# Kernel tuning notes

Measured on AMD Instinct MI355X. Metric: run time of the kernel, lower is better.

The kernel has to match this reference:

```python
import jax, jax.numpy as jnp
import numpy as np

N_NODES = 100000
N_EDGES = 1600000
N_FEAT = 128
N_HID = 128
N_CLASS = 10
N_GRAPHS = 512
BN_EPS = 1e-5


def setup_inputs() -> dict:
    key = jax.random.key(0)
    ks = jax.random.split(key, 12)
    x = jax.random.normal(ks[0], (N_NODES, N_FEAT), dtype=jnp.float32)
    edge_index = jax.random.randint(ks[1], (2, N_EDGES), 0, N_NODES, dtype=jnp.int32)
    batch = jnp.sort(jax.random.randint(ks[2], (N_NODES,), 0, N_GRAPHS, dtype=jnp.int32))
    s1 = 1.0 / np.sqrt(N_FEAT)
    s2 = 1.0 / np.sqrt(N_HID)
    W1 = jax.random.uniform(ks[3], (N_FEAT, N_HID), jnp.float32, -s1, s1)
    b1 = jax.random.uniform(ks[4], (N_HID,), jnp.float32, -s1, s1)
    gamma = jnp.ones((N_HID,), jnp.float32)
    beta = jnp.zeros((N_HID,), jnp.float32)
    W2 = jax.random.uniform(ks[5], (N_HID, N_HID), jnp.float32, -s2, s2)
    b2 = jax.random.uniform(ks[6], (N_HID,), jnp.float32, -s2, s2)
    clsW = jax.random.uniform(ks[7], (N_HID, N_CLASS), jnp.float32, -s2, s2)
    clsb = jax.random.uniform(ks[8], (N_CLASS,), jnp.float32, -s2, s2)
    return {"x": x, "edge_index": edge_index, "batch": batch,
            "W1": W1, "b1": b1, "gamma": gamma, "beta": beta,
            "W2": W2, "b2": b2, "clsW": clsW, "clsb": clsb}


def _gcn_norm(edge_index, n_nodes):
    # add self-loops, compute symmetric normalization D^-1/2 A_hat D^-1/2
    loops = jnp.arange(n_nodes, dtype=edge_index.dtype)
    src = jnp.concatenate([edge_index[0], loops])
    dst = jnp.concatenate([edge_index[1], loops])
    deg = jax.ops.segment_sum(jnp.ones_like(dst, dtype=jnp.float32), dst,
                              num_segments=n_nodes)
    dinv = jnp.where(deg > 0, jax.lax.rsqrt(deg), 0.0)
    norm = dinv[src] * dinv[dst]  # [E + N]
    return src, dst, norm


def _gcn_conv(h, src, dst, norm, W, b, n_nodes):
    h = h @ W                                   # [N, nhid] dense GEMM
    msg = h[src] * norm[:, None]                # gather + scale  [E+N, nhid]
    out = jax.ops.segment_sum(msg, dst, num_segments=n_nodes)  # scatter-add
    return out + b


def reference(x, edge_index, batch, W1, b1, gamma, beta, W2, b2, clsW, clsb):
    n_nodes = x.shape[0]
    src, dst, norm = _gcn_norm(edge_index, n_nodes)
    # layer 1: GCNConv -> BatchNorm(eval, running stats 0/1) -> ReLU -> Dropout(eval=id)
    h = _gcn_conv(x, src, dst, norm, W1, b1, n_nodes)
    h = h * (gamma / jnp.sqrt(1.0 + BN_EPS)) + beta
    h = jax.nn.relu(h)
    # layer 2: GCNConv (output layer, no bn/act)
    h = _gcn_conv(h, src, dst, norm, W2, b2, n_nodes)
    # global mean pool over batch index
    sums = jax.ops.segment_sum(h, batch, num_segments=N_GRAPHS)          # [G, nhid]
    cnts = jax.ops.segment_sum(jnp.ones((n_nodes,), h.dtype), batch,
                               num_segments=N_GRAPHS)
    g = sums / jnp.maximum(cnts, 1.0)[:, None]
    out = jax.nn.log_softmax(g @ clsW + clsb, axis=1)                    # [G, nclass]
    return out, g
```

## Files before the change

kernel.cpp:

```cpp
#include <hip/hip_runtime.h>
#include <hip/hip_bf16.h>

#define N_NODES 100000
#define N_EDGES 1600000
#define N_FEAT 128
#define N_HID 128
#define N_CLASS 10
#define N_GRAPHS 512
#define BN_RSQRT 0.9999950000374997f

#define NRANGE 12500
#define NSUB 512
#define SCAP 640
#define HGROUP 32
#define BPB (NSUB / HGROUP)

#define XT_STRIDE 136
#define XT_BYTES (64 * XT_STRIDE * 2)
#define YW_STRIDE 36

typedef _Float16 half_t;
typedef __attribute__((ext_vector_type(2))) _Float16 half2v;
typedef __attribute__((ext_vector_type(4))) _Float16 half4v;
typedef __attribute__((ext_vector_type(8))) _Float16 half8v;
typedef __attribute__((ext_vector_type(4))) float floatx4;
typedef __attribute__((ext_vector_type(2))) float floatx2;

__global__ __launch_bounds__(256) void bucket_fused(
    const int* __restrict__ src, const int* __restrict__ dst,
    int* __restrict__ cnt, unsigned long long* __restrict__ bucketed,
    const float* __restrict__ W1, half_t* __restrict__ Wt1,
    const float* __restrict__ W2, half_t* __restrict__ Wt2,
    const int* __restrict__ batch, int* __restrict__ boffs,
    int chunkE, int E, int nnodes)
{
    __shared__ int wcnt[4][8];
    __shared__ int wbase[4][8];
    int blk = blockIdx.x;
    if (blk >= NSUB) {
        int k = blk - NSUB;
        if (k < 128) {
            int i = k * 256 + threadIdx.x;
            const float* W = (i < 16384) ? W1 : W2;
            half_t* Wt = (i < 16384) ? Wt1 : Wt2;
            int j = i & 16383;
            int c = j >> 7, kk = j & 127;
            Wt[(size_t)c * 128 + kk] = (half_t)W[(size_t)kk * 128 + c];
        } else {
            int i = (k - 128) * 256 + threadIdx.x;
            if (i < nnodes) {
                int b = batch[i];
                int prev = (i == 0) ? -1 : batch[i - 1];
                for (int g = prev + 1; g <= b; ++g) boffs[g] = i;
                if (i == nnodes - 1)
                    for (int g = b + 1; g <= N_GRAPHS; ++g) boffs[g] = nnodes;
            }
        }
        return;
    }
    int b = blk;
    int wave = threadIdx.x >> 6;
    int lane = threadIdx.x & 63;
    int e0 = b * chunkE;
    int e1 = e0 + chunkE < E ? e0 + chunkE : E;
    int iters = (chunkE + 255) / 256;

    int mycnt = 0;
    for (int it = 0; it < iters; ++it) {
        int e = e0 + it * 256 + threadIdx.x;
        bool valid = e < e1;
        int d = valid ? dst[e] : 0;
        int rr = (d * 8) / N_NODES;
#pragma unroll
        for (int r = 0; r < 8; ++r) {
            unsigned long long m = __ballot(valid && rr == r);
            if (lane == r) mycnt += __popcll(m);
        }
    }
    if (lane < 8) wcnt[wave][lane] = mycnt;
    __syncthreads();
    if (threadIdx.x < 8) {
        int r = threadIdx.x;
        int s = 0;
#pragma unroll
        for (int w = 0; w < 4; ++w) { wbase[w][r] = s; s += wcnt[w][r]; }
        cnt[r * NSUB + b] = s;
    }
    __syncthreads();

    int myoff = (lane < 8) ? wbase[wave][lane] : 0;
    for (int it = 0; it < iters; ++it) {
        int e = e0 + it * 256 + threadIdx.x;
        bool valid = e < e1;
        int s = valid ? src[e] : 0;
        int d = valid ? dst[e] : 0;
        int rr = (d * 8) / N_NODES;
        unsigned long long pk = ((unsigned long long)(unsigned)d << 32) | (unsigned)s;
#pragma unroll
        for (int r = 0; r < 8; ++r) {
            unsigned long long m = __ballot(valid && rr == r);
            int base_r = __shfl(myoff, r);
            if (valid && rr == r) {
                int pos = base_r + __popcll(m & ((1ull << lane) - 1));
                if (pos < SCAP)
                    bucketed[(size_t)(r * NSUB + b) * SCAP + pos] = pk;
            }
            if (lane == r) myoff += __popcll(m);
        }
    }
}

__global__ __launch_bounds__(256) void hist2(
    const unsigned long long* __restrict__ bucketed, const int* __restrict__ cnt,
    int* __restrict__ partial)
{
    __shared__ int h[NRANGE];
    int r = blockIdx.x & 7, g = blockIdx.x >> 3;
    for (int i = threadIdx.x; i < NRANGE; i += 256) h[i] = 0;
    __syncthreads();
    int rbase = r * NRANGE;
    for (int j = 0; j < BPB; ++j) {
        int b = g * BPB + j;
        int n = cnt[r * NSUB + b];
        if (n > SCAP) n = SCAP;
        const unsigned long long* seg = bucketed + (size_t)(r * NSUB + b) * SCAP;
        for (int i = threadIdx.x; i < n; i += 256)
            atomicAdd(&h[(int)(seg[i] >> 32) - rbase], 1);
    }
    __syncthreads();
    int* slice = partial + (size_t)(r * HGROUP + g) * NRANGE;
    for (int i = threadIdx.x; i < NRANGE; i += 256) slice[i] = h[i];
}

__global__ void deg_reduce(const int* __restrict__ partial, int* __restrict__ deg,
                           float* __restrict__ dinv, int* __restrict__ bsums, int n) {
    __shared__ int sm[256];
    int t = threadIdx.x;
    int i = blockIdx.x * 256 + t;
    int s = 0;
    if (i < n) {
        int rr = i / NRANGE;
        int dl = i - rr * NRANGE;
        const int* p = partial + (size_t)rr * HGROUP * NRANGE + dl;
#pragma unroll 8
        for (int g = 0; g < HGROUP; ++g) s += p[(size_t)g * NRANGE];
        deg[i] = s;
        dinv[i] = rsqrtf((float)s + 1.0f);
    }
    sm[t] = s;
    __syncthreads();
    for (int off = 128; off > 0; off >>= 1) {
        if (t < off) sm[t] += sm[t + off];
        __syncthreads();
    }
    if (t == 0) bsums[blockIdx.x] = sm[0];
}

__global__ void scan_small(int* __restrict__ bsums, int nb) {
    __shared__ int buf[1024];
    int t = threadIdx.x;
    int v = (t < nb) ? bsums[t] : 0;
    buf[t] = v;
    __syncthreads();
    for (int off = 1; off < 1024; off <<= 1) {
        int x = (t >= off) ? buf[t - off] : 0;
        __syncthreads();
        buf[t] += x;
        __syncthreads();
    }
    if (t < nb) bsums[t] = buf[t] - v;
}

__global__ __launch_bounds__(256) void scan_chunkoff(
    const int* __restrict__ in, const int* __restrict__ bsums,
    int* __restrict__ rowptr, int* __restrict__ partial, int n, int total)
{
    __shared__ int s[256];
    int t = threadIdx.x;
    int i = blockIdx.x * 256 + t;
    int v = (i < n) ? in[i] : 0;
    s[t] = v;
    __syncthreads();
    for (int off = 1; off < 256; off <<= 1) {
        int x = (t >= off) ? s[t - off] : 0;
        __syncthreads();
        s[t] += x;
        __syncthreads();
    }
    if (i == 0) rowptr[n] = total;
    if (i < n) {
        int excl = bsums[blockIdx.x] + s[t] - v;
        rowptr[i] = excl;
        int rr = i / NRANGE;
        int dl = i - rr * NRANGE;
        int* p = partial + (size_t)rr * HGROUP * NRANGE + dl;
        int vals[32];
#pragma unroll
        for (int g = 0; g < 32; ++g) vals[g] = p[(size_t)g * NRANGE];
        int running = excl;
#pragma unroll
        for (int g = 0; g < 32; ++g) {
            int tmp = vals[g];
            p[(size_t)g * NRANGE] = running;
            running += tmp;
        }
    }
}

__global__ __launch_bounds__(256, 4) void gemm1_mfma(
    const float* __restrict__ X, const half_t* __restrict__ Wt,
    const float* __restrict__ dinv, unsigned char* __restrict__ Y8, int nrows)
{
    __shared__ __align__(16) unsigned char smem[XT_BYTES];
    int tid = threadIdx.x;
    int r0base = blockIdx.x * 64;
    half_t* xt = (half_t*)smem;
    {
        const float4* xg = (const float4*)(X + (size_t)r0base * 128);
        if (r0base + 64 <= nrows) {
            float4 f[8];
#pragma unroll
            for (int j = 0; j < 8; ++j) f[j] = xg[j * 256 + tid];
#pragma unroll
            for (int j = 0; j < 8; ++j) {
                int idx = j * 256 + tid;
                int row = idx >> 5;
                int c4 = (idx & 31) << 2;
                half4v h = {(half_t)f[j].x, (half_t)f[j].y, (half_t)f[j].z, (half_t)f[j].w};
                *(half4v*)(xt + row * XT_STRIDE + c4) = h;
            }
        } else {
            int idxmax = (nrows - r0base) * 32;
#pragma unroll
            for (int j = 0; j < 8; ++j) {
                int idx = j * 256 + tid;
                if (idx < idxmax) {
                    float4 f = xg[idx];
                    int row = idx >> 5;
                    int c4 = (idx & 31) << 2;
                    half4v h = {(half_t)f.x, (half_t)f.y, (half_t)f.z, (half_t)f.w};
                    *(half4v*)(xt + row * XT_STRIDE + c4) = h;
                }
            }
        }
    }
    __syncthreads();
    int wave = tid >> 6;
    int lane = tid & 63;
    int n16  = lane & 15;
    int quad = lane >> 4;
    int r0 = r0base + wave * 16;
    bool active = r0 < nrows;
    int packedv[8];
    if (active) {
        int row = r0 + n16;
        const half_t* xr = xt + (wave * 16 + n16) * XT_STRIDE;
        half8v a0 = *(const half8v*)(xr + 0 * 32 + quad * 8);
        half8v a1 = *(const half8v*)(xr + 1 * 32 + quad * 8);
        half8v a2 = *(const half8v*)(xr + 2 * 32 + quad * 8);
        half8v a3 = *(const half8v*)(xr + 3 * 32 + quad * 8);
        float dr = dinv[row];
#pragma unroll
        for (int c = 0; c < 8; ++c) {
            const half8v* wrow = (const half8v*)(Wt + (size_t)(c * 16 + n16) * 128);
            floatx4 acc = {0.f, 0.f, 0.f, 0.f};
            acc = __builtin_amdgcn_mfma_f32_16x16x32_f16(wrow[0 * 4 + quad], a0, acc, 0, 0, 0);
            acc = __builtin_amdgcn_mfma_f32_16x16x32_f16(wrow[1 * 4 + quad], a1, acc, 0, 0, 0);
            acc = __builtin_amdgcn_mfma_f32_16x16x32_f16(wrow[2 * 4 + quad], a2, acc, 0, 0, 0);
            acc = __builtin_amdgcn_mfma_f32_16x16x32_f16(wrow[3 * 4 + quad], a3, acc, 0, 0, 0);
            int packed = __builtin_amdgcn_cvt_pk_fp8_f32(acc[0] * dr, acc[1] * dr, 0, false);
            packed = __builtin_amdgcn_cvt_pk_fp8_f32(acc[2] * dr, acc[3] * dr, packed, true);
            packedv[c] = packed;
        }
    }
    __syncthreads();
    int* yw = (int*)smem + wave * (16 * YW_STRIDE);
    if (active) {
#pragma unroll
        for (int c = 0; c < 8; ++c)
            yw[n16 * YW_STRIDE + c * 4 + quad] = packedv[c];
#pragma unroll
        for (int t = 0; t < 2; ++t) {
            int4 v = *(const int4*)(yw + (t * 8 + (lane >> 3)) * YW_STRIDE + (lane & 7) * 4);
            *(int4*)(Y8 + (size_t)r0 * 128 + t * 1024 + lane * 16) = v;
        }
    }
}

__global__ __launch_bounds__(256) void fill2(
    const unsigned long long* __restrict__ bucketed, const int* __restrict__ cnt,
    const int* __restrict__ partial, int* __restrict__ col)
{
    __shared__ int off[NRANGE];
    int r = blockIdx.x & 7, g = blockIdx.x >> 3;
    const int* slice = partial + (size_t)(r * HGROUP + g) * NRANGE;
    for (int i = threadIdx.x; i < NRANGE; i += 256) off[i] = slice[i];
    __syncthreads();
    int rbase = r * NRANGE;
    for (int j = 0; j < BPB; ++j) {
        int b = g * BPB + j;
        int n = cnt[r * NSUB + b];
        if (n > SCAP) n = SCAP;
        const unsigned long long* seg = bucketed + (size_t)(r * NSUB + b) * SCAP;
        for (int i = threadIdx.x; i < n; i += 256) {
            unsigned long long pk = seg[i];
            int pos = atomicAdd(&off[(int)(pk >> 32) - rbase], 1);
            col[pos] = (int)((unsigned)(pk & 0xffffffffu) << 7);
        }
    }
}

__global__ __launch_bounds__(256, 4) void gemm2_mfma(
    const half_t* __restrict__ X, const half_t* __restrict__ Wt,
    const float* __restrict__ dinv, unsigned char* __restrict__ Y8, int nrows)
{
    __shared__ __align__(16) unsigned char smem[XT_BYTES];
    int tid = threadIdx.x;
    int r0base = blockIdx.x * 64;
    half_t* xt = (half_t*)smem;
    {
        const half8v* xg = (const half8v*)(X + (size_t)r0base * 128);
        if (r0base + 64 <= nrows) {
            half8v v[4];
#pragma unroll
            for (int j = 0; j < 4; ++j) v[j] = xg[j * 256 + tid];
#pragma unroll
            for (int j = 0; j < 4; ++j) {
                int idx = j * 256 + tid;
                int row = idx >> 4;
                int sub = (idx & 15) << 3;
                *(half8v*)(xt + row * XT_STRIDE + sub) = v[j];
            }
        } else {
            int idxmax = (nrows - r0base) * 16;
#pragma unroll
            for (int j = 0; j < 4; ++j) {
                int idx = j * 256 + tid;
                if (idx < idxmax) {
                    half8v v = xg[idx];
                    int row = idx >> 4;
                    int sub = (idx & 15) << 3;
                    *(half8v*)(xt + row * XT_STRIDE + sub) = v;
                }
            }
        }
    }
    __syncthreads();
    int wave = tid >> 6;
    int lane = tid & 63;
    int n16  = lane & 15;
    int quad = lane >> 4;
    int r0 = r0base + wave * 16;
    bool active = r0 < nrows;
    int packedv[8];
    if (active) {
        int row = r0 + n16;
        const half_t* xr = xt + (wave * 16 + n16) * XT_STRIDE;
        half8v a0 = *(const half8v*)(xr + 0 * 32 + quad * 8);
        half8v a1 = *(const half8v*)(xr + 1 * 32 + quad * 8);
        half8v a2 = *(const half8v*)(xr + 2 * 32 + quad * 8);
        half8v a3 = *(const half8v*)(xr + 3 * 32 + quad * 8);
        float dr = dinv[row];
#pragma unroll
        for (int c = 0; c < 8; ++c) {
            const half8v* wrow = (const half8v*)(Wt + (size_t)(c * 16 + n16) * 128);
            floatx4 acc = {0.f, 0.f, 0.f, 0.f};
            acc = __builtin_amdgcn_mfma_f32_16x16x32_f16(wrow[0 * 4 + quad], a0, acc, 0, 0, 0);
            acc = __builtin_amdgcn_mfma_f32_16x16x32_f16(wrow[1 * 4 + quad], a1, acc, 0, 0, 0);
            acc = __builtin_amdgcn_mfma_f32_16x16x32_f16(wrow[2 * 4 + quad], a2, acc, 0, 0, 0);
            acc = __builtin_amdgcn_mfma_f32_16x16x32_f16(wrow[3 * 4 + quad], a3, acc, 0, 0, 0);
            int packed = __builtin_amdgcn_cvt_pk_fp8_f32(acc[0] * dr, acc[1] * dr, 0, false);
            packed = __builtin_amdgcn_cvt_pk_fp8_f32(acc[2] * dr, acc[3] * dr, packed, true);
            packedv[c] = packed;
        }
    }
    __syncthreads();
    int* yw = (int*)smem + wave * (16 * YW_STRIDE);
    if (active) {
#pragma unroll
        for (int c = 0; c < 8; ++c)
            yw[n16 * YW_STRIDE + c * 4 + quad] = packedv[c];
#pragma unroll
        for (int t = 0; t < 2; ++t) {
            int4 v = *(const int4*)(yw + (t * 8 + (lane >> 3)) * YW_STRIDE + (lane & 7) * 4);
            *(int4*)(Y8 + (size_t)r0 * 128 + t * 1024 + lane * 16) = v;
        }
    }
}

__global__ __launch_bounds__(256, 4) void agg_fp8(
    const unsigned char* __restrict__ hs, half_t* __restrict__ out,
    const int* __restrict__ col, const int* __restrict__ rowptr,
    const float* __restrict__ bias,
    const float* __restrict__ gamma, const float* __restrict__ beta,
    int nnodes, int do_bn_relu)
{
    int wave = threadIdx.x >> 6;
    int lane = threadIdx.x & 63;
    int q = lane >> 4;
    int l16 = lane & 15;
    int nb4 = (blockIdx.x * 4 + wave) * 4;
    int i = nb4 + q;
    bool valid = i < nnodes;
    unsigned iq = valid ? (unsigned)i : (unsigned)nnodes;
    unsigned f8 = (unsigned)l16 << 3;
    unsigned ZOFF = (unsigned)nnodes << 7;

    int e0 = valid ? rowptr[i] : 0;
    int e1 = valid ? rowptr[i + 1] : 0;
    int deg = e1 - e0;
    int m = deg;
    m = max(m, __shfl_xor(m, 16));
    m = max(m, __shfl_xor(m, 32));
    int nchunk = (m + 15) >> 4;

    unsigned long long us = *(const unsigned long long*)(hs + ((iq << 7) | f8));

    floatx2 a0 = {0.f, 0.f}, a1 = {0.f, 0.f}, a2 = {0.f, 0.f}, a3 = {0.f, 0.f};
    for (int t = 0; t < nchunk; ++t) {
        int idx = e0 + t * 16 + l16;
        unsigned cv = (idx < e1) ? (unsigned)col[idx] : ZOFF;
#pragma unroll
        for (int half = 0; half < 2; ++half) {
            const int kk = half * 8;
            unsigned long long v0, v1, v2, v3, v4, v5, v6, v7;
#define AGG_ADDR(K)                                                            \
            ({ unsigned sA = (unsigned)__builtin_amdgcn_readlane((int)cv, kk + K);      \
               unsigned sB = (unsigned)__builtin_amdgcn_readlane((int)cv, kk + K + 16); \
               unsigned sC = (unsigned)__builtin_amdgcn_readlane((int)cv, kk + K + 32); \
               unsigned sD = (unsigned)__builtin_amdgcn_readlane((int)cv, kk + K + 48); \
               unsigned rAB = (q & 1) ? sB : sA;                               \
               unsigned rCD = (q & 1) ? sD : sC;                               \
               unsigned rr = (q & 2) ? rCD : rAB;                              \
               *(const unsigned long long*)(hs + (rr | f8)); })
            v0 = AGG_ADDR(0);
            v1 = AGG_ADDR(1);
            v2 = AGG_ADDR(2);
            v3 = AGG_ADDR(3);
            v4 = AGG_ADDR(4);
            v5 = AGG_ADDR(5);
            v6 = AGG_ADDR(6);
            v7 = AGG_ADDR(7);
#undef AGG_ADDR
#define AGG_ACC(V)                                                             \
            { unsigned lo = (unsigned)(V), hi = (unsigned)((V) >> 32);         \
              a0 += __builtin_amdgcn_cvt_pk_f32_fp8((int)lo, false);           \
              a1 += __builtin_amdgcn_cvt_pk_f32_fp8((int)lo, true);            \
              a2 += __builtin_amdgcn_cvt_pk_f32_fp8((int)hi, false);           \
              a3 += __builtin_amdgcn_cvt_pk_f32_fp8((int)hi, true); }
            AGG_ACC(v0) AGG_ACC(v1) AGG_ACC(v2) AGG_ACC(v3)
            AGG_ACC(v4) AGG_ACC(v5) AGG_ACC(v6) AGG_ACC(v7)
#undef AGG_ACC
        }
    }
    {
        unsigned lo = (unsigned)us, hi = (unsigned)(us >> 32);
        a0 += __builtin_amdgcn_cvt_pk_f32_fp8((int)lo, false);
        a1 += __builtin_amdgcn_cvt_pk_f32_fp8((int)lo, true);
        a2 += __builtin_amdgcn_cvt_pk_f32_fp8((int)hi, false);
        a3 += __builtin_amdgcn_cvt_pk_f32_fp8((int)hi, true);
    }

    if (!valid) return;
    float di = rsqrtf((float)deg + 1.0f);
    int fbase = l16 * 8;
    float4 bi0 = *(const float4*)(bias + fbase);
    float4 bi1 = *(const float4*)(bias + fbase + 4);
    float o0 = fmaf(di, a0.x, bi0.x);
    float o1 = fmaf(di, a0.y, bi0.y);
    float o2 = fmaf(di, a1.x, bi0.z);
    float o3 = fmaf(di, a1.y, bi0.w);
    float o4 = fmaf(di, a2.x, bi1.x);
    float o5 = fmaf(di, a2.y, bi1.y);
    float o6 = fmaf(di, a3.x, bi1.z);
    float o7 = fmaf(di, a3.y, bi1.w);
    if (do_bn_relu) {
        float4 ga0 = *(const float4*)(gamma + fbase);
        float4 ga1 = *(const float4*)(gamma + fbase + 4);
        float4 be0 = *(const float4*)(beta + fbase);
        float4 be1 = *(const float4*)(beta + fbase + 4);
        o0 = fmaf(o0, ga0.x * BN_RSQRT, be0.x);
        o1 = fmaf(o1, ga0.y * BN_RSQRT, be0.y);
        o2 = fmaf(o2, ga0.z * BN_RSQRT, be0.z);
        o3 = fmaf(o3, ga0.w * BN_RSQRT, be0.w);
        o4 = fmaf(o4, ga1.x * BN_RSQRT, be1.x);
        o5 = fmaf(o5, ga1.y * BN_RSQRT, be1.y);
        o6 = fmaf(o6, ga1.z * BN_RSQRT, be1.z);
        o7 = fmaf(o7, ga1.w * BN_RSQRT, be1.w);
        o0 = o0 > 0.f ? o0 : 0.f;
        o1 = o1 > 0.f ? o1 : 0.f;
        o2 = o2 > 0.f ? o2 : 0.f;
        o3 = o3 > 0.f ? o3 : 0.f;
        o4 = o4 > 0.f ? o4 : 0.f;
        o5 = o5 > 0.f ? o5 : 0.f;
        o6 = o6 > 0.f ? o6 : 0.f;
        o7 = o7 > 0.f ? o7 : 0.f;
    }
    half8v ov = {(half_t)o0, (half_t)o1, (half_t)o2, (half_t)o3,
                 (half_t)o4, (half_t)o5, (half_t)o6, (half_t)o7};
    *(half8v*)(out + (size_t)i * 128 + fbase) = ov;
}

__global__ __launch_bounds__(512) void pool_cls(
    const half_t* __restrict__ h, const int* __restrict__ boffs,
    const float* __restrict__ clsW, const float* __restrict__ clsb,
    float* __restrict__ gout, float* __restrict__ out)
{
    __shared__ float red[8][128];
    __shared__ float zbuf[16];
    int g = blockIdx.x;
    int w = threadIdx.x >> 6;
    int lane = threadIdx.x & 63;
    int n0 = boffs[g], n1 = boffs[g + 1];
    float ax = 0.f, ay = 0.f;
    for (int n = n0 + w; n < n1; n += 8) {
        half2v v = *(const half2v*)(h + (size_t)n * 128 + lane * 2);
        ax += (float)v.x;
        ay += (float)v.y;
    }
    red[w][lane * 2] = ax;
    red[w][lane * 2 + 1] = ay;
    __syncthreads();
    if (w == 0) {
        float sx = 0.f, sy = 0.f;
#pragma unroll
        for (int j = 0; j < 8; ++j) {
            sx += red[j][lane * 2];
            sy += red[j][lane * 2 + 1];
        }
        float cnt = (float)((n1 - n0) > 1 ? (n1 - n0) : 1);
        float g0 = sx / cnt, g1 = sy / cnt;
        gout[(size_t)g * 128 + lane * 2] = g0;
        gout[(size_t)g * 128 + lane * 2 + 1] = g1;
        red[0][lane * 2] = g0;
        red[0][lane * 2 + 1] = g1;
    }
    __syncthreads();
    if (threadIdx.x < N_CLASS) {
        int c = threadIdx.x;
        float z = clsb[c];
        for (int k = 0; k < N_HID; ++k)
            z = fmaf(red[0][k], clsW[k * N_CLASS + c], z);
        zbuf[c] = z;
    }
    __syncthreads();
    if (threadIdx.x == 0) {
        float m = zbuf[0];
#pragma unroll
        for (int c = 1; c < N_CLASS; ++c) m = fmaxf(m, zbuf[c]);
        float s = 0.f;
#pragma unroll
        for (int c = 0; c < N_CLASS; ++c) s += expf(zbuf[c] - m);
        float l = logf(s);
#pragma unroll
        for (int c = 0; c < N_CLASS; ++c)
            out[(size_t)g * N_CLASS + c] = zbuf[c] - m - l;
    }
}

extern "C" void kernel_launch(void* const* d_in, const int* in_sizes, int n_in,
                              void* d_out, int out_size, void* d_ws, size_t ws_size,
                              hipStream_t stream) {
    const float* x     = (const float*)d_in[0];
    const int*   ei    = (const int*)d_in[1];
    const int*   batch = (const int*)d_in[2];
    const float* W1    = (const float*)d_in[3];
    const float* b1    = (const float*)d_in[4];
    const float* gamma = (const float*)d_in[5];
    const float* beta  = (const float*)d_in[6];
    const float* W2    = (const float*)d_in[7];
    const float* b2    = (const float*)d_in[8];
    const float* clsW  = (const float*)d_in[9];
    const float* clsb  = (const float*)d_in[10];

    const int N = in_sizes[0] / N_FEAT;
    const int E = in_sizes[1] / 2;
    const int* src = ei;
    const int* dst = ei + E;

    unsigned char* BA8 = (unsigned char*)d_ws;
    half_t* BB = (half_t*)(BA8 + (size_t)(N + 1) * 128);
    half_t* Wt1 = BB + (size_t)N * 128;
    half_t* Wt2 = Wt1 + 16384;
    int*   col     = (int*)(Wt2 + 16384);
    int*   rowptr  = col + E;
    int*   deg     = rowptr + (N + 4);
    float* dinv    = (float*)(deg + N);
    int*   cnt     = (int*)(dinv + N);
    unsigned long long* bucketed =
        (unsigned long long*)(cnt + 8 * NSUB);
    int*   partial = (int*)(bucketed + (size_t)8 * NSUB * SCAP);
    int*   boffs   = partial + 8 * HGROUP * NRANGE;
    int*   bsums   = boffs + N_GRAPHS + 4;

    const int nb = (N + 255) / 256;
    const int chunkE = (E + NSUB - 1) / NSUB;
    const int gemmBlocks = (N + 63) / 64;
    const int aggBlocks = (N + 15) / 16;

    hipMemsetAsync(BA8 + (size_t)N * 128, 0, 128, stream);

    bucket_fused<<<NSUB + 128 + nb, 256, 0, stream>>>(
        src, dst, cnt, bucketed, W1, Wt1, W2, Wt2, batch, boffs, chunkE, E, N);
    hist2<<<8 * HGROUP, 256, 0, stream>>>(bucketed, cnt, partial);
    deg_reduce<<<nb, 256, 0, stream>>>(partial, deg, dinv, bsums, N);
    scan_small<<<1, 1024, 0, stream>>>(bsums, nb);
    scan_chunkoff<<<nb, 256, 0, stream>>>(deg, bsums, rowptr, partial, N, E);
    gemm1_mfma<<<gemmBlocks, 256, 0, stream>>>(x, Wt1, dinv, BA8, N);
    fill2<<<256, 256, 0, stream>>>(bucketed, cnt, partial, col);
    agg_fp8<<<aggBlocks, 256, 0, stream>>>(BA8, BB, col, rowptr, b1, gamma, beta, N, 1);
    gemm2_mfma<<<gemmBlocks, 256, 0, stream>>>(BB, Wt2, dinv, BA8, N);
    agg_fp8<<<aggBlocks, 256, 0, stream>>>(BA8, BB, col, rowptr, b2, gamma, beta, N, 0);

    float* out = (float*)d_out;
    float* gsec = out + (size_t)N_GRAPHS * N_CLASS;
    pool_cls<<<N_GRAPHS, 512, 0, stream>>>(BB, boffs, clsW, clsb, gsec, out);
}
```

Baseline: 313.9 us.

## Replace bucketed CSR build with global atomic degree count and atomic fill

Drops the multi-pass bucket/histogram/partial-offset CSR construction. Degrees are now counted with global atomics on dst, and col is filled by atomically bumping per-node cursors. This removes the intermediate bucketed buffer and two kernels, plus their LDS histogram passes. In exchange it uses 1.6M global atomics twice with random addresses, and the order of neighbours within a row is no longer deterministic, so fp accumulation order may vary between runs.

```diff
diff --git a/kernel.cpp b/kernel.cpp
--- a/kernel.cpp
+++ b/kernel.cpp
@@ -9,12 +9,6 @@
 #define N_GRAPHS 512
 #define BN_RSQRT 0.9999950000374997f
 
-#define NRANGE 12500
-#define NSUB 512
-#define SCAP 640
-#define HGROUP 32
-#define BPB (NSUB / HGROUP)
-
 #define XT_STRIDE 136
 #define XT_BYTES (64 * XT_STRIDE * 2)
 #define YW_STRIDE 36
@@ -26,125 +20,55 @@
 typedef __attribute__((ext_vector_type(4))) float floatx4;
 typedef __attribute__((ext_vector_type(2))) float floatx2;
 
-__global__ __launch_bounds__(256) void bucket_fused(
-    const int* __restrict__ src, const int* __restrict__ dst,
-    int* __restrict__ cnt, unsigned long long* __restrict__ bucketed,
+__global__ __launch_bounds__(256) void count_fused(
+    const int* __restrict__ dst, int* __restrict__ deg,
     const float* __restrict__ W1, half_t* __restrict__ Wt1,
     const float* __restrict__ W2, half_t* __restrict__ Wt2,
     const int* __restrict__ batch, int* __restrict__ boffs,
-    int chunkE, int E, int nnodes)
-{
-    __shared__ int wcnt[4][8];
-    __shared__ int wbase[4][8];
+    int E, int nnodes, int EB)
+{
     int blk = blockIdx.x;
-    if (blk >= NSUB) {
-        int k = blk - NSUB;
-        if (k < 128) {
-            int i = k * 256 + threadIdx.x;
-            const float* W = (i < 16384) ? W1 : W2;
-            half_t* Wt = (i < 16384) ? Wt1 : Wt2;
-            int j = i & 16383;
-            int c = j >> 7, kk = j & 127;
-            Wt[(size_t)c * 128 + kk] = (half_t)W[(size_t)kk * 128 + c];
-        } else {
-            int i = (k - 128) * 256 + threadIdx.x;
-            if (i < nnodes) {
-                int b = batch[i];
-                int prev = (i == 0) ? -1 : batch[i - 1];
-                for (int g = prev + 1; g <= b; ++g) boffs[g] = i;
-                if (i == nnodes - 1)
-                    for (int g = b + 1; g <= N_GRAPHS; ++g) boffs[g] = nnodes;
-            }
+    if (blk < EB) {
+        int e4 = (blk * 256 + threadIdx.x) * 4;
+        if (e4 < E) {
+            int4 d4 = *(const int4*)(dst + e4);
+            atomicAdd(&deg[d4.x], 1);
+            atomicAdd(&deg[d4.y], 1);
+            atomicAdd(&deg[d4.z], 1);
+            atomicAdd(&deg[d4.w], 1);
         }
         return;
     }
-    int b = blk;
-    int wave = threadIdx.x >> 6;
-    int lane = threadIdx.x & 63;
-    int e0 = b * chunkE;
-    int e1 = e0 + chunkE < E ? e0 + chunkE : E;
-    int iters = (chunkE + 255) / 256;
-
-    int mycnt = 0;
-    for (int it = 0; it < iters; ++it) {
-        int e = e0 + it * 256 + threadIdx.x;
-        bool valid = e < e1;
-        int d = valid ? dst[e] : 0;
-        int rr = (d * 8) / N_NODES;
-#pragma unroll
-        for (int r = 0; r < 8; ++r) {
-            unsigned long long m = __ballot(valid && rr == r);
-            if (lane == r) mycnt += __popcll(m);
-        }
-    }
-    if (lane < 8) wcnt[wave][lane] = mycnt;
-    __syncthreads();
-    if (threadIdx.x < 8) {
-        int r = threadIdx.x;
-        int s = 0;
-#pragma unroll
-        for (int w = 0; w < 4; ++w) { wbase[w][r] = s; s += wcnt[w][r]; }
-        cnt[r * NSUB + b] = s;
-    }
-    __syncthreads();
-
-    int myoff = (lane < 8) ? wbase[wave][lane] : 0;
-    for (int it = 0; it < iters; ++it) {
-        int e = e0 + it * 256 + threadIdx.x;
-        bool valid = e < e1;
-        int s = valid ? src[e] : 0;
-        int d = valid ? dst[e] : 0;
-        int rr = (d * 8) / N_NODES;
-        unsigned long long pk = ((unsigned long long)(unsigned)d << 32) | (unsigned)s;
-#pragma unroll
-        for (int r = 0; r < 8; ++r) {
-            unsigned long long m = __ballot(valid && rr == r);
-            int base_r = __shfl(myoff, r);
-            if (valid && rr == r) {
-                int pos = base_r + __popcll(m & ((1ull << lane) - 1));
-                if (pos < SCAP)
-                    bucketed[(size_t)(r * NSUB + b) * SCAP + pos] = pk;
-            }
-            if (lane == r) myoff += __popcll(m);
-        }
-    }
-}
-
-__global__ __launch_bounds__(256) void hist2(
-    const unsigned long long* __restrict__ bucketed, const int* __restrict__ cnt,
-    int* __restrict__ partial)
-{
-    __shared__ int h[NRANGE];
-    int r = blockIdx.x & 7, g = blockIdx.x >> 3;
-    for (int i = threadIdx.x; i < NRANGE; i += 256) h[i] = 0;
-    __syncthreads();
-    int rbase = r * NRANGE;
-    for (int j = 0; j < BPB; ++j) {
-        int b = g * BPB + j;
-        int n = cnt[r * NSUB + b];
-        if (n > SCAP) n = SCAP;
-        const unsigned long long* seg = bucketed + (size_t)(r * NSUB + b) * SCAP;
-        for (int i = threadIdx.x; i < n; i += 256)
-            atomicAdd(&h[(int)(seg[i] >> 32) - rbase], 1);
-    }
-    __syncthreads();
-    int* slice = partial + (size_t)(r * HGROUP + g) * NRANGE;
-    for (int i = threadIdx.x; i < NRANGE; i += 256) slice[i] = h[i];
-}
-
-__global__ void deg_reduce(const int* __restrict__ partial, int* __restrict__ deg,
-                           float* __restrict__ dinv, int* __restrict__ bsums, int n) {
+    int k = blk - EB;
+    if (k < 128) {
+        int i = k * 256 + threadIdx.x;
+        const float* W = (i < 16384) ? W1 : W2;
+        half_t* Wt = (i < 16384) ? Wt1 : Wt2;
+        int j = i & 16383;
+        int c = j >> 7, kk = j & 127;
+        Wt[(size_t)c * 128 + kk] = (half_t)W[(size_t)kk * 128 + c];
+    } else {
+        int i = (k - 128) * 256 + threadIdx.x;
+        if (i < nnodes) {
+            int b = batch[i];
+            int prev = (i == 0) ? -1 : batch[i - 1];
+            for (int g = prev + 1; g <= b; ++g) boffs[g] = i;
+            if (i == nnodes - 1)
+                for (int g = b + 1; g <= N_GRAPHS; ++g) boffs[g] = nnodes;
+        }
+    }
+}
+
+__global__ __launch_bounds__(256) void dinv_bsums(
+    const int* __restrict__ deg, float* __restrict__ dinv,
+    int* __restrict__ bsums, int n)
+{
     __shared__ int sm[256];
     int t = threadIdx.x;
     int i = blockIdx.x * 256 + t;
     int s = 0;
     if (i < n) {
-        int rr = i / NRANGE;
-        int dl = i - rr * NRANGE;
-        const int* p = partial + (size_t)rr * HGROUP * NRANGE + dl;
-#pragma unroll 8
-        for (int g = 0; g < HGROUP; ++g) s += p[(size_t)g * NRANGE];
-        deg[i] = s;
+        s = deg[i];
         dinv[i] = rsqrtf((float)s + 1.0f);
     }
     sm[t] = s;
@@ -171,9 +95,9 @@
     if (t < nb) bsums[t] = buf[t] - v;
 }
 
-__global__ __launch_bounds__(256) void scan_chunkoff(
+__global__ __launch_bounds__(256) void scan_final_cursor(
     const int* __restrict__ in, const int* __restrict__ bsums,
-    int* __restrict__ rowptr, int* __restrict__ partial, int n, int total)
+    int* __restrict__ rowptr, int* __restrict__ cursor, int n, int total)
 {
     __shared__ int s[256];
     int t = threadIdx.x;
@@ -191,20 +115,26 @@
     if (i < n) {
         int excl = bsums[blockIdx.x] + s[t] - v;
         rowptr[i] = excl;
-        int rr = i / NRANGE;
-        int dl = i - rr * NRANGE;
-        int* p = partial + (size_t)rr * HGROUP * NRANGE + dl;
-        int vals[32];
-#pragma unroll
-        for (int g = 0; g < 32; ++g) vals[g] = p[(size_t)g * NRANGE];
-        int running = excl;
-#pragma unroll
-        for (int g = 0; g < 32; ++g) {
-            int tmp = vals[g];
-            p[(size_t)g * NRANGE] = running;
-            running += tmp;
-        }
-    }
+        cursor[i] = excl;
+    }
+}
+
+__global__ __launch_bounds__(256) void fill_atomic(
+    const int* __restrict__ src, const int* __restrict__ dst,
+    int* __restrict__ cursor, int* __restrict__ col, int E)
+{
+    int e4 = (blockIdx.x * 256 + threadIdx.x) * 4;
+    if (e4 >= E) return;
+    int4 s4 = *(const int4*)(src + e4);
+    int4 d4 = *(const int4*)(dst + e4);
+    int p0 = atomicAdd(&cursor[d4.x], 1);
+    int p1 = atomicAdd(&cursor[d4.y], 1);
+    int p2 = atomicAdd(&cursor[d4.z], 1);
+    int p3 = atomicAdd(&cursor[d4.w], 1);
+    col[p0] = s4.x << 7;
+    col[p1] = s4.y << 7;
+    col[p2] = s4.z << 7;
+    col[p3] = s4.w << 7;
 }
 
 __global__ __launch_bounds__(256, 4) void gemm1_mfma(
@@ -283,29 +213,6 @@
         for (int t = 0; t < 2; ++t) {
             int4 v = *(const int4*)(yw + (t * 8 + (lane >> 3)) * YW_STRIDE + (lane & 7) * 4);
             *(int4*)(Y8 + (size_t)r0 * 128 + t * 1024 + lane * 16) = v;
-        }
-    }
-}
-
-__global__ __launch_bounds__(256) void fill2(
-    const unsigned long long* __restrict__ bucketed, const int* __restrict__ cnt,
-    const int* __restrict__ partial, int* __restrict__ col)
-{
-    __shared__ int off[NRANGE];
-    int r = blockIdx.x & 7, g = blockIdx.x >> 3;
-    const int* slice = partial + (size_t)(r * HGROUP + g) * NRANGE;
-    for (int i = threadIdx.x; i < NRANGE; i += 256) off[i] = slice[i];
-    __syncthreads();
-    int rbase = r * NRANGE;
-    for (int j = 0; j < BPB; ++j) {
-        int b = g * BPB + j;
-        int n = cnt[r * NSUB + b];
-        if (n > SCAP) n = SCAP;
-        const unsigned long long* seg = bucketed + (size_t)(r * NSUB + b) * SCAP;
-        for (int i = threadIdx.x; i < n; i += 256) {
-            unsigned long long pk = seg[i];
-            int pos = atomicAdd(&off[(int)(pk >> 32) - rbase], 1);
-            col[pos] = (int)((unsigned)(pk & 0xffffffffu) << 7);
         }
     }
 }
@@ -586,28 +493,25 @@
     int*   rowptr  = col + E;
     int*   deg     = rowptr + (N + 4);
     float* dinv    = (float*)(deg + N);
-    int*   cnt     = (int*)(dinv + N);
-    unsigned long long* bucketed =
-        (unsigned long long*)(cnt + 8 * NSUB);
-    int*   partial = (int*)(bucketed + (size_t)8 * NSUB * SCAP);
-    int*   boffs   = partial + 8 * HGROUP * NRANGE;
+    int*   cursor  = (int*)(dinv + N);
+    int*   boffs   = cursor + N;
     int*   bsums   = boffs + N_GRAPHS + 4;
 
     const int nb = (N + 255) / 256;
-    const int chunkE = (E + NSUB - 1) / NSUB;
+    const int EB = (E / 4 + 255) / 256;
     const int gemmBlocks = (N + 63) / 64;
     const int aggBlocks = (N + 15) / 16;
 
     hipMemsetAsync(BA8 + (size_t)N * 128, 0, 128, stream);
-
-    bucket_fused<<<NSUB + 128 + nb, 256, 0, stream>>>(
-        src, dst, cnt, bucketed, W1, Wt1, W2, Wt2, batch, boffs, chunkE, E, N);
-    hist2<<<8 * HGROUP, 256, 0, stream>>>(bucketed, cnt, partial);
-    deg_reduce<<<nb, 256, 0, stream>>>(partial, deg, dinv, bsums, N);
+    hipMemsetAsync(deg, 0, (size_t)N * sizeof(int), stream);
+
+    count_fused<<<EB + 128 + nb, 256, 0, stream>>>(
+        dst, deg, W1, Wt1, W2, Wt2, batch, boffs, E, N, EB);
+    dinv_bsums<<<nb, 256, 0, stream>>>(deg, dinv, bsums, N);
     scan_small<<<1, 1024, 0, stream>>>(bsums, nb);
-    scan_chunkoff<<<nb, 256, 0, stream>>>(deg, bsums, rowptr, partial, N, E);
+    scan_final_cursor<<<nb, 256, 0, stream>>>(deg, bsums, rowptr, cursor, N, E);
+    fill_atomic<<<EB, 256, 0, stream>>>(src, dst, cursor, col, E);
     gemm1_mfma<<<gemmBlocks, 256, 0, stream>>>(x, Wt1, dinv, BA8, N);
-    fill2<<<256, 256, 0, stream>>>(bucketed, cnt, partial, col);
     agg_fp8<<<aggBlocks, 256, 0, stream>>>(BA8, BB, col, rowptr, b1, gamma, beta, N, 1);
     gemm2_mfma<<<gemmBlocks, 256, 0, stream>>>(BB, Wt2, dinv, BA8, N);
     agg_fp8<<<aggBlocks, 256, 0, stream>>>(BA8, BB, col, rowptr, b2, gamma, beta, N, 0);
```

New measurement: 462.4 us. +47.3%, slower.

## Make GEMM kernels persistent with LDS-resident weights and double-buffered row tiles

Applied to the files above, without the earlier changes.

Both dense GEMM kernels become persistent: a fixed grid of 512 blocks loops over the 64-row tiles. Each block stages the transposed weight matrix in LDS once. It then prefetches the next tile's rows into registers while running MFMA on the current tile, using two LDS tile buffers. This targets repeated global weight fetches and per-block launch and load latency, at the cost of higher LDS use (launch bounds drop to 2 blocks) and extra barriers per tile.

```diff
diff --git a/kernel.cpp b/kernel.cpp
--- a/kernel.cpp
+++ b/kernel.cpp
@@ -16,7 +16,6 @@
 #define BPB (NSUB / HGROUP)
 
 #define XT_STRIDE 136
-#define XT_BYTES (64 * XT_STRIDE * 2)
 #define YW_STRIDE 36
 
 typedef _Float16 half_t;
@@ -207,86 +206,6 @@
     }
 }
 
-__global__ __launch_bounds__(256, 4) void gemm1_mfma(
-    const float* __restrict__ X, const half_t* __restrict__ Wt,
-    const float* __restrict__ dinv, unsigned char* __restrict__ Y8, int nrows)
-{
-    __shared__ __align__(16) unsigned char smem[XT_BYTES];
-    int tid = threadIdx.x;
-    int r0base = blockIdx.x * 64;
-    half_t* xt = (half_t*)smem;
-    {
-        const float4* xg = (const float4*)(X + (size_t)r0base * 128);
-        if (r0base + 64 <= nrows) {
-            float4 f[8];
-#pragma unroll
-            for (int j = 0; j < 8; ++j) f[j] = xg[j * 256 + tid];
-#pragma unroll
-            for (int j = 0; j < 8; ++j) {
-                int idx = j * 256 + tid;
-                int row = idx >> 5;
-                int c4 = (idx & 31) << 2;
-                half4v h = {(half_t)f[j].x, (half_t)f[j].y, (half_t)f[j].z, (half_t)f[j].w};
-                *(half4v*)(xt + row * XT_STRIDE + c4) = h;
-            }
-        } else {
-            int idxmax = (nrows - r0base) * 32;
-#pragma unroll
-            for (int j = 0; j < 8; ++j) {
-                int idx = j * 256 + tid;
-                if (idx < idxmax) {
-                    float4 f = xg[idx];
-                    int row = idx >> 5;
-                    int c4 = (idx & 31) << 2;
-                    half4v h = {(half_t)f.x, (half_t)f.y, (half_t)f.z, (half_t)f.w};
-                    *(half4v*)(xt + row * XT_STRIDE + c4) = h;
-                }
-            }
-        }
-    }
-    __syncthreads();
-    int wave = tid >> 6;
-    int lane = tid & 63;
-    int n16  = lane & 15;
-    int quad = lane >> 4;
-    int r0 = r0base + wave * 16;
-    bool active = r0 < nrows;
-    int packedv[8];
-    if (active) {
-        int row = r0 + n16;
-        const half_t* xr = xt + (wave * 16 + n16) * XT_STRIDE;
-        half8v a0 = *(const half8v*)(xr + 0 * 32 + quad * 8);
-        half8v a1 = *(const half8v*)(xr + 1 * 32 + quad * 8);
-        half8v a2 = *(const half8v*)(xr + 2 * 32 + quad * 8);
-        half8v a3 = *(const half8v*)(xr + 3 * 32 + quad * 8);
-        float dr = dinv[row];
-#pragma unroll
-        for (int c = 0; c < 8; ++c) {
-            const half8v* wrow = (const half8v*)(Wt + (size_t)(c * 16 + n16) * 128);
-            floatx4 acc = {0.f, 0.f, 0.f, 0.f};
-            acc = __builtin_amdgcn_mfma_f32_16x16x32_f16(wrow[0 * 4 + quad], a0, acc, 0, 0, 0);
-            acc = __builtin_amdgcn_mfma_f32_16x16x32_f16(wrow[1 * 4 + quad], a1, acc, 0, 0, 0);
-            acc = __builtin_amdgcn_mfma_f32_16x16x32_f16(wrow[2 * 4 + quad], a2, acc, 0, 0, 0);
-            acc = __builtin_amdgcn_mfma_f32_16x16x32_f16(wrow[3 * 4 + quad], a3, acc, 0, 0, 0);
-            int packed = __builtin_amdgcn_cvt_pk_fp8_f32(acc[0] * dr, acc[1] * dr, 0, false);
-            packed = __builtin_amdgcn_cvt_pk_fp8_f32(acc[2] * dr, acc[3] * dr, packed, true);
-            packedv[c] = packed;
-        }
-    }
-    __syncthreads();
-    int* yw = (int*)smem + wave * (16 * YW_STRIDE);
-    if (active) {
-#pragma unroll
-        for (int c = 0; c < 8; ++c)
-            yw[n16 * YW_STRIDE + c * 4 + quad] = packedv[c];
-#pragma unroll
-        for (int t = 0; t < 2; ++t) {
-            int4 v = *(const int4*)(yw + (t * 8 + (lane >> 3)) * YW_STRIDE + (lane & 7) * 4);
-            *(int4*)(Y8 + (size_t)r0 * 128 + t * 1024 + lane * 16) = v;
-        }
-    }
-}
-
 __global__ __launch_bounds__(256) void fill2(
     const unsigned long long* __restrict__ bucketed, const int* __restrict__ cnt,
     const int* __restrict__ partial, int* __restrict__ col)
@@ -310,81 +229,210 @@
     }
 }
 
-__global__ __launch_bounds__(256, 4) void gemm2_mfma(
-    const half_t* __restrict__ X, const half_t* __restrict__ Wt,
-    const float* __restrict__ dinv, unsigned char* __restrict__ Y8, int nrows)
-{
-    __shared__ __align__(16) unsigned char smem[XT_BYTES];
+__global__ __launch_bounds__(256, 2) void gemm1_mfma(
+    const float* __restrict__ X, const half_t* __restrict__ Wt,
+    const float* __restrict__ dinv, unsigned char* __restrict__ Y8,
+    int nrows, int ntiles)
+{
+    __shared__ __align__(16) half_t wlds[128 * XT_STRIDE];
+    __shared__ __align__(16) half_t xb[2][64 * XT_STRIDE];
+    __shared__ __align__(16) int yw_all[4 * 16 * YW_STRIDE];
     int tid = threadIdx.x;
-    int r0base = blockIdx.x * 64;
-    half_t* xt = (half_t*)smem;
     {
-        const half8v* xg = (const half8v*)(X + (size_t)r0base * 128);
-        if (r0base + 64 <= nrows) {
-            half8v v[4];
-#pragma unroll
-            for (int j = 0; j < 4; ++j) v[j] = xg[j * 256 + tid];
-#pragma unroll
-            for (int j = 0; j < 4; ++j) {
-                int idx = j * 256 + tid;
-                int row = idx >> 4;
-                int sub = (idx & 15) << 3;
-                *(half8v*)(xt + row * XT_STRIDE + sub) = v[j];
-            }
-        } else {
-            int idxmax = (nrows - r0base) * 16;
-#pragma unroll
-            for (int j = 0; j < 4; ++j) {
-                int idx = j * 256 + tid;
-                if (idx < idxmax) {
-                    half8v v = xg[idx];
-                    int row = idx >> 4;
-                    int sub = (idx & 15) << 3;
-                    *(half8v*)(xt + row * XT_STRIDE + sub) = v;
-                }
-            }
-        }
-    }
-    __syncthreads();
+        const half8v* wg = (const half8v*)Wt;
+        half8v w[8];
+#pragma unroll
+        for (int j = 0; j < 8; ++j) w[j] = wg[j * 256 + tid];
+#pragma unroll
+        for (int j = 0; j < 8; ++j) {
+            int idx = j * 256 + tid;
+            *(half8v*)(wlds + (idx >> 4) * XT_STRIDE + ((idx & 15) << 3)) = w[j];
+        }
+    }
     int wave = tid >> 6;
     int lane = tid & 63;
     int n16  = lane & 15;
     int quad = lane >> 4;
-    int r0 = r0base + wave * 16;
-    bool active = r0 < nrows;
-    int packedv[8];
-    if (active) {
-        int row = r0 + n16;
-        const half_t* xr = xt + (wave * 16 + n16) * XT_STRIDE;
-        half8v a0 = *(const half8v*)(xr + 0 * 32 + quad * 8);
-        half8v a1 = *(const half8v*)(xr + 1 * 32 + quad * 8);
-        half8v a2 = *(const half8v*)(xr + 2 * 32 + quad * 8);
-        half8v a3 = *(const half8v*)(xr + 3 * 32 + quad * 8);
-        float dr = dinv[row];
-#pragma unroll
-        for (int c = 0; c < 8; ++c) {
-            const half8v* wrow = (const half8v*)(Wt + (size_t)(c * 16 + n16) * 128);
-            floatx4 acc = {0.f, 0.f, 0.f, 0.f};
-            acc = __builtin_amdgcn_mfma_f32_16x16x32_f16(wrow[0 * 4 + quad], a0, acc, 0, 0, 0);
-            acc = __builtin_amdgcn_mfma_f32_16x16x32_f16(wrow[1 * 4 + quad], a1, acc, 0, 0, 0);
-            acc = __builtin_amdgcn_mfma_f32_16x16x32_f16(wrow[2 * 4 + quad], a2, acc, 0, 0, 0);
-            acc = __builtin_amdgcn_mfma_f32_16x16x32_f16(wrow[3 * 4 + quad], a3, acc, 0, 0, 0);
-            int packed = __builtin_amdgcn_cvt_pk_fp8_f32(acc[0] * dr, acc[1] * dr, 0, false);
-            packed = __builtin_amdgcn_cvt_pk_fp8_f32(acc[2] * dr, acc[3] * dr, packed, true);
-            packedv[c] = packed;
-        }
-    }
-    __syncthreads();
-    int* yw = (int*)smem + wave * (16 * YW_STRIDE);
-    if (active) {
-#pragma unroll
-        for (int c = 0; c < 8; ++c)
-            yw[n16 * YW_STRIDE + c * 4 + quad] = packedv[c];
-#pragma unroll
-        for (int t = 0; t < 2; ++t) {
-            int4 v = *(const int4*)(yw + (t * 8 + (lane >> 3)) * YW_STRIDE + (lane & 7) * 4);
-            *(int4*)(Y8 + (size_t)r0 * 128 + t * 1024 + lane * 16) = v;
-        }
+    int* yw = yw_all + wave * (16 * YW_STRIDE);
+
+    int t = blockIdx.x;
+    if (t >= ntiles) return;
+    int cur = 0;
+    {
+        const float4* xg = (const float4*)(X + (size_t)t * 64 * 128);
+        int idxmax = (nrows - t * 64) * 32;
+#pragma unroll
+        for (int j = 0; j < 8; ++j) {
+            int idx = j * 256 + tid;
+            if (idx < idxmax) {
+                float4 f = xg[idx];
+                half4v h = {(half_t)f.x, (half_t)f.y, (half_t)f.z, (half_t)f.w};
+                *(half4v*)(xb[0] + (idx >> 5) * XT_STRIDE + ((idx & 31) << 2)) = h;
+            }
+        }
+    }
+    __syncthreads();
+    for (;;) {
+        int tn = t + gridDim.x;
+        bool pf = tn < ntiles;
+        float4 f[8];
+        if (pf) {
+            const float4* xg = (const float4*)(X + (size_t)tn * 64 * 128);
+            int idxmax = (nrows - tn * 64) * 32;
+#pragma unroll
+            for (int j = 0; j < 8; ++j) {
+                int idx = j * 256 + tid;
+                f[j] = (idx < idxmax) ? xg[idx] : float4{0.f, 0.f, 0.f, 0.f};
+            }
+        }
+        int r0 = t * 64 + wave * 16;
+        bool active = r0 < nrows;
+        int packedv[8];
+        if (active) {
+            const half_t* xr = xb[cur] + (wave * 16 + n16) * XT_STRIDE;
+            half8v a0 = *(const half8v*)(xr + 0 * 32 + quad * 8);
+            half8v a1 = *(const half8v*)(xr + 1 * 32 + quad * 8);
+            half8v a2 = *(const half8v*)(xr + 2 * 32 + quad * 8);
+            half8v a3 = *(const half8v*)(xr + 3 * 32 + quad * 8);
+            float dr = dinv[r0 + n16];
+#pragma unroll
+            for (int c = 0; c < 8; ++c) {
+                const half_t* wl = wlds + (c * 16 + n16) * XT_STRIDE;
+                floatx4 acc = {0.f, 0.f, 0.f, 0.f};
+                acc = __builtin_amdgcn_mfma_f32_16x16x32_f16(*(const half8v*)(wl + 0 * 32 + quad * 8), a0, acc, 0, 0, 0);
+                acc = __builtin_amdgcn_mfma_f32_16x16x32_f16(*(const half8v*)(wl + 1 * 32 + quad * 8), a1, acc, 0, 0, 0);
+                acc = __builtin_amdgcn_mfma_f32_16x16x32_f16(*(const half8v*)(wl + 2 * 32 + quad * 8), a2, acc, 0, 0, 0);
+                acc = __builtin_amdgcn_mfma_f32_16x16x32_f16(*(const half8v*)(wl + 3 * 32 + quad * 8), a3, acc, 0, 0, 0);
+                int packed = __builtin_amdgcn_cvt_pk_fp8_f32(acc[0] * dr, acc[1] * dr, 0, false);
+                packed = __builtin_amdgcn_cvt_pk_fp8_f32(acc[2] * dr, acc[3] * dr, packed, true);
+                packedv[c] = packed;
+            }
+#pragma unroll
+            for (int c = 0; c < 8; ++c)
+                yw[n16 * YW_STRIDE + c * 4 + quad] = packedv[c];
+#pragma unroll
+            for (int u = 0; u < 2; ++u) {
+                int4 v = *(const int4*)(yw + (u * 8 + (lane >> 3)) * YW_STRIDE + (lane & 7) * 4);
+                *(int4*)(Y8 + (size_t)r0 * 128 + u * 1024 + lane * 16) = v;
+            }
+        }
+        __syncthreads();
+        if (!pf) break;
+        {
+            int idxmax = (nrows - tn * 64) * 32;
+#pragma unroll
+            for (int j = 0; j < 8; ++j) {
+                int idx = j * 256 + tid;
+                if (idx < idxmax) {
+                    half4v h = {(half_t)f[j].x, (half_t)f[j].y, (half_t)f[j].z, (half_t)f[j].w};
+                    *(half4v*)(xb[cur ^ 1] + (idx >> 5) * XT_STRIDE + ((idx & 31) << 2)) = h;
+                }
+            }
+        }
+        __syncthreads();
+        cur ^= 1;
+        t = tn;
+    }
+}
+
+__global__ __launch_bounds__(256, 2) void gemm2_mfma(
+    const half_t* __restrict__ X, const half_t* __restrict__ Wt,
+    const float* __restrict__ dinv, unsigned char* __restrict__ Y8,
+    int nrows, int ntiles)
+{
+    __shared__ __align__(16) half_t wlds[128 * XT_STRIDE];
+    __shared__ __align__(16) half_t xb[2][64 * XT_STRIDE];
+    __shared__ __align__(16) int yw_all[4 * 16 * YW_STRIDE];
+    int tid = threadIdx.x;
+    {
+        const half8v* wg = (const half8v*)Wt;
+        half8v w[8];
+#pragma unroll
+        for (int j = 0; j < 8; ++j) w[j] = wg[j * 256 + tid];
+#pragma unroll
+        for (int j = 0; j < 8; ++j) {
+            int idx = j * 256 + tid;
+            *(half8v*)(wlds + (idx >> 4) * XT_STRIDE + ((idx & 15) << 3)) = w[j];
+        }
+    }
+    int wave = tid >> 6;
+    int lane = tid & 63;
+    int n16  = lane & 15;
+    int quad = lane >> 4;
+    int* yw = yw_all + wave * (16 * YW_STRIDE);
+
+    int t = blockIdx.x;
+    if (t >= ntiles) return;
+    int cur = 0;
+    {
+        const half8v* xg = (const half8v*)(X + (size_t)t * 64 * 128);
+        int idxmax = (nrows - t * 64) * 16;
+#pragma unroll
+        for (int j = 0; j < 4; ++j) {
+            int idx = j * 256 + tid;
+            if (idx < idxmax)
+                *(half8v*)(xb[0] + (idx >> 4) * XT_STRIDE + ((idx & 15) << 3)) = xg[idx];
+        }
+    }
+    __syncthreads();
+    for (;;) {
+        int tn = t + gridDim.x;
+        bool pf = tn < ntiles;
+        half8v v[4];
+        if (pf) {
+            const half8v* xg = (const half8v*)(X + (size_t)tn * 64 * 128);
+            int idxmax = (nrows - tn * 64) * 16;
+#pragma unroll
+            for (int j = 0; j < 4; ++j) {
+                int idx = j * 256 + tid;
+                if (idx < idxmax) v[j] = xg[idx];
+            }
+        }
+        int r0 = t * 64 + wave * 16;
+        bool active = r0 < nrows;
+        int packedv[8];
+        if (active) {
+            const half_t* xr = xb[cur] + (wave * 16 + n16) * XT_STRIDE;
+            half8v a0 = *(const half8v*)(xr + 0 * 32 + quad * 8);
+            half8v a1 = *(const half8v*)(xr + 1 * 32 + quad * 8);
+            half8v a2 = *(const half8v*)(xr + 2 * 32 + quad * 8);
+            half8v a3 = *(const half8v*)(xr + 3 * 32 + quad * 8);
+            float dr = dinv[r0 + n16];
+#pragma unroll
+            for (int c = 0; c < 8; ++c) {
+                const half_t* wl = wlds + (c * 16 + n16) * XT_STRIDE;
+                floatx4 acc = {0.f, 0.f, 0.f, 0.f};
+                acc = __builtin_amdgcn_mfma_f32_16x16x32_f16(*(const half8v*)(wl + 0 * 32 + quad * 8), a0, acc, 0, 0, 0);
+                acc = __builtin_amdgcn_mfma_f32_16x16x32_f16(*(const half8v*)(wl + 1 * 32 + quad * 8), a1, acc, 0, 0, 0);
+                acc = __builtin_amdgcn_mfma_f32_16x16x32_f16(*(const half8v*)(wl + 2 * 32 + quad * 8), a2, acc, 0, 0, 0);
+                acc = __builtin_amdgcn_mfma_f32_16x16x32_f16(*(const half8v*)(wl + 3 * 32 + quad * 8), a3, acc, 0, 0, 0);
+                int packed = __builtin_amdgcn_cvt_pk_fp8_f32(acc[0] * dr, acc[1] * dr, 0, false);
+                packed = __builtin_amdgcn_cvt_pk_fp8_f32(acc[2] * dr, acc[3] * dr, packed, true);
+                packedv[c] = packed;
+            }
+#pragma unroll
+            for (int c = 0; c < 8; ++c)
+                yw[n16 * YW_STRIDE + c * 4 + quad] = packedv[c];
+#pragma unroll
+            for (int u = 0; u < 2; ++u) {
+                int4 o = *(const int4*)(yw + (u * 8 + (lane >> 3)) * YW_STRIDE + (lane & 7) * 4);
+                *(int4*)(Y8 + (size_t)r0 * 128 + u * 1024 + lane * 16) = o;
+            }
+        }
+        __syncthreads();
+        if (!pf) break;
+        {
+            int idxmax = (nrows - tn * 64) * 16;
+#pragma unroll
+            for (int j = 0; j < 4; ++j) {
+                int idx = j * 256 + tid;
+                if (idx < idxmax)
+                    *(half8v*)(xb[cur ^ 1] + (idx >> 4) * XT_STRIDE + ((idx & 15) << 3)) = v[j];
+            }
+        }
+        __syncthreads();
+        cur ^= 1;
+        t = tn;
     }
 }
 
@@ -595,7 +643,8 @@
 
     const int nb = (N + 255) / 256;
     const int chunkE = (E + NSUB - 1) / NSUB;
-    const int gemmBlocks = (N + 63) / 64;
+    const int ntiles = (N + 63) / 64;
+    const int gemmGrid = 512;
     const int aggBlocks = (N + 15) / 16;
 
     hipMemsetAsync(BA8 + (size_t)N * 128, 0, 128, stream);
@@ -606,10 +655,10 @@
     deg_reduce<<<nb, 256, 0, stream>>>(partial, deg, dinv, bsums, N);
     scan_small<<<1, 1024, 0, stream>>>(bsums, nb);
     scan_chunkoff<<<nb, 256, 0, stream>>>(deg, bsums, rowptr, partial, N, E);
-    gemm1_mfma<<<gemmBlocks, 256, 0, stream>>>(x, Wt1, dinv, BA8, N);
+    gemm1_mfma<<<gemmGrid, 256, 0, stream>>>(x, Wt1, dinv, BA8, N, ntiles);
     fill2<<<256, 256, 0, stream>>>(bucketed, cnt, partial, col);
     agg_fp8<<<aggBlocks, 256, 0, stream>>>(BA8, BB, col, rowptr, b1, gamma, beta, N, 1);
-    gemm2_mfma<<<gemmBlocks, 256, 0, stream>>>(BB, Wt2, dinv, BA8, N);
+    gemm2_mfma<<<gemmGrid, 256, 0, stream>>>(BB, Wt2, dinv, BA8, N, ntiles);
     agg_fp8<<<aggBlocks, 256, 0, stream>>>(BA8, BB, col, rowptr, b2, gamma, beta, N, 0);
 
     float* out = (float*)d_out;
```

Result: faster. 286.5 us (-8.7%).
